# Kernel tuning notes

Measured on AMD Instinct MI355X. Metric: run time of the kernel, lower is better.

## Reference

```python
import jax, jax.numpy as jnp
import numpy as np

N = 100000
E = 800000
D_IN = 64
D_OUT = 64
SCALES = (4, 8)


def setup_inputs() -> dict:
    key = jax.random.key(0)
    ks = jax.random.split(key, 8)
    x = jax.random.normal(ks[0], (N, D_IN), dtype=jnp.float32)
    edge_index = jax.random.randint(ks[1], (2, E), 0, N, dtype=jnp.int64)
    s = 1.0 / np.sqrt(D_IN)
    W1 = jax.random.uniform(ks[2], (D_OUT, D_IN), minval=-s, maxval=s, dtype=jnp.float32)
    b1 = jax.random.uniform(ks[3], (D_OUT,), minval=-s, maxval=s, dtype=jnp.float32)
    W2 = jax.random.uniform(ks[4], (D_OUT, D_IN), minval=-s, maxval=s, dtype=jnp.float32)
    b2 = jax.random.uniform(ks[5], (D_OUT,), minval=-s, maxval=s, dtype=jnp.float32)
    sg = 1.0 / np.sqrt(D_OUT * len(SCALES))
    Wg = jax.random.uniform(ks[6], (D_OUT, D_OUT * len(SCALES)), minval=-sg, maxval=sg, dtype=jnp.float32)
    bg = jax.random.uniform(ks[7], (D_OUT,), minval=-sg, maxval=sg, dtype=jnp.float32)
    return {"x": x, "edge_index": edge_index, "W1": W1, "b1": b1,
            "W2": W2, "b2": b2, "Wg": Wg, "bg": bg}


def _gconv(x, src, tgt, W, b):
    # scatter-add neighbor features: agg[src] += x[tgt]
    agg = jax.ops.segment_sum(x[tgt], src, num_segments=N)  # [N, D_IN]
    counts = jax.ops.segment_sum(jnp.ones((src.shape[0], 1), x.dtype), src,
                                 num_segments=N) + 1e-6     # [N, 1]
    agg = agg / counts
    return agg @ W.T + b                                    # [N, D_OUT]


def reference(x, edge_index, W1, b1, W2, b2, Wg, bg):
    k_max = E // N  # = 8
    outs = []
    for scale, (W, b) in zip(SCALES, ((W1, b1), (W2, b2))):
        scale = min(scale, k_max)
        src = edge_index[0, :N * scale]
        tgt = edge_index[1, :N * scale]
        outs.append(_gconv(x, src, tgt, W, b))
    multi = jnp.concatenate(outs, axis=-1)                   # [N, 2*D_OUT]
    gate = jax.nn.sigmoid(multi @ Wg.T + bg)                 # [N, D_OUT]
    fused = gate * outs[0] + (1.0 - gate) * outs[1]
    return fused
```

## Files before the change

kernel.cpp:

```cpp
#include <hip/hip_runtime.h>
#include <hip/hip_bf16.h>

#define N_NODES 100000
#define E_TOTAL 800000
#define E1      400000
#define D       64
#define CAP     32

#define NPB        128
#define NB         ((N_NODES + NPB - 1) / NPB)
#define BSTRIDE    (NPB * CAP)
#define BCAP       1536
#define EPB        2048
#define NBKT_BLKS  ((E_TOTAL + EPB - 1) / EPB)
#define PREP_TPB   512
#define EPT        (EPB / PREP_TPB)

typedef short s16x8 __attribute__((ext_vector_type(8)));
typedef float f32x4 __attribute__((ext_vector_type(4)));
typedef unsigned u32x4 __attribute__((ext_vector_type(4)));

#define WS_CNT     0
#define WS_ENTRIES (N_NODES)
#define WS_W1B     (WS_ENTRIES + N_NODES * CAP)
#define WS_W2B     (WS_W1B + 2048)
#define WS_WGB     (WS_W2B + 2048)
#define WS_BIAS    (WS_WGB + 4096)
#define WS_CUR     (WS_BIAS + 192)

#define PREP_CONV_BLOCKS 5

__device__ __forceinline__ float ldv(const void* p, size_t idx, int fp32)
{
    return fp32 ? ((const float*)p)[idx]
                : __bfloat162float(((const __hip_bfloat16*)p)[idx]);
}

__device__ __forceinline__ void detect2(const int* ei, const unsigned short* xu,
                                        int* s2, int& e64, int& fp32)
{
    if (threadIdx.x == 0) { s2[0] = 0; s2[1] = 0; }
    __syncthreads();
    if (threadIdx.x < 16 && ei[2 * threadIdx.x + 1] != 0) atomicOr(&s2[0], 1);
    { unsigned u = xu[threadIdx.x]; if (((u >> 7) & 0xFF) >= 0x90) atomicOr(&s2[1], 1); }
    __syncthreads();
    e64 = (s2[0] == 0); fp32 = s2[1];
}

__global__ __launch_bounds__(512) void prep_kernel(
    const void* __restrict__ xv, const int* __restrict__ ei,
    const void* __restrict__ W1v, const void* __restrict__ b1v,
    const void* __restrict__ W2v, const void* __restrict__ b2v,
    const void* __restrict__ Wgv, const void* __restrict__ bgv,
    unsigned* __restrict__ ws)
{
    __shared__ int s2[2];
    __shared__ unsigned hist[NB];
    __shared__ unsigned bbase[NB];
    int e64, fp32;
    detect2(ei, (const unsigned short*)xv, s2, e64, fp32);

    if (blockIdx.x < NBKT_BLKS) {
        for (int j = threadIdx.x; j < NB; j += PREP_TPB) hist[j] = 0;
        __syncthreads();

        const int e0 = blockIdx.x * EPB;
        int srcv[EPT], tgtv[EPT];
#pragma unroll
        for (int i = 0; i < EPT; ++i) {
            const int e = e0 + i * PREP_TPB + threadIdx.x;
            srcv[i] = -1;
            if (e < E_TOTAL) {
                if (e64) {
                    srcv[i] = (int)((const uint2*)ei)[e].x;
                    tgtv[i] = (int)((const uint2*)ei)[E_TOTAL + e].x;
                } else {
                    srcv[i] = ei[e]; tgtv[i] = ei[E_TOTAL + e];
                }
            }
        }
        unsigned recv[EPT], br[EPT];
#pragma unroll
        for (int i = 0; i < EPT; ++i) {
            const int e = e0 + i * PREP_TPB + threadIdx.x;
            br[i] = 0xFFFFFFFFu;
            if (srcv[i] >= 0) {
                const unsigned b = (unsigned)srcv[i] >> 7;
                const unsigned r = atomicAdd(&hist[b], 1u);
                recv[i] = (unsigned)tgtv[i]
                        | ((e < E1) ? 0x20000u : 0u)
                        | (((unsigned)srcv[i] & (NPB - 1)) << 18);
                br[i] = (b << 16) | r;
            }
        }
        __syncthreads();
        for (int j = threadIdx.x; j < NB; j += PREP_TPB) {
            const unsigned h = hist[j];
            bbase[j] = h ? atomicAdd(ws + WS_CUR + j, h) : 0u;
        }
        __syncthreads();
#pragma unroll
        for (int i = 0; i < EPT; ++i) {
            if (br[i] != 0xFFFFFFFFu) {
                const unsigned b = br[i] >> 16, r = br[i] & 0xFFFFu;
                const unsigned pos = bbase[b] + r;
                if (pos < BCAP)
                    ws[WS_ENTRIES + (size_t)b * BSTRIDE + pos] = recv[i];
            }
        }
        return;
    }

    const int gid = (blockIdx.x - NBKT_BLKS) * PREP_TPB + threadIdx.x;
    __hip_bfloat16* W1b = (__hip_bfloat16*)(ws + WS_W1B);
    __hip_bfloat16* W2b = (__hip_bfloat16*)(ws + WS_W2B);
    __hip_bfloat16* Wgb = (__hip_bfloat16*)(ws + WS_WGB);
    float* bias = (float*)(ws + WS_BIAS);

    if (gid < 2048) {
#pragma unroll
        for (int k = 0; k < 8; ++k) {
            const int i = gid * 8 + k;
            if (i < 4096)       W1b[i]        = __float2bfloat16(ldv(W1v, i, fp32));
            else if (i < 8192)  W2b[i - 4096] = __float2bfloat16(ldv(W2v, i - 4096, fp32));
            else                Wgb[i - 8192] = __float2bfloat16(ldv(Wgv, i - 8192, fp32));
        }
    } else if (gid < 2072) {
        const int j = gid - 2048;
#pragma unroll
        for (int k = 0; k < 8; ++k) {
            const int i = j * 8 + k;
            if (i < 64)       bias[i] = ldv(b1v, i, fp32);
            else if (i < 128) bias[i] = ldv(b2v, i - 64, fp32);
            else              bias[i] = ldv(bgv, i - 128, fp32);
        }
    }
}

__global__ __launch_bounds__(256) void csr_kernel(unsigned* __restrict__ ws)
{
    __shared__ unsigned rec_s[BCAP];
    __shared__ __align__(16) unsigned ent[NPB * CAP];
    __shared__ unsigned n1c[NPB], ctc[NPB], a1[NPB], a2[NPB];

    const int b  = blockIdx.x;
    const int n0 = b * NPB;
    const int nn = min(NPB, N_NODES - n0);

    for (int j = threadIdx.x; j < NPB; j += 256) { n1c[j] = 0; ctc[j] = 0; }
    {
        const u32x4 z = {0u, 0u, 0u, 0u};
        for (int j = threadIdx.x; j < NPB * CAP / 4; j += 256) ((u32x4*)ent)[j] = z;
    }
    const unsigned C = min(ws[WS_CUR + b], (unsigned)BCAP);
    for (unsigned r = threadIdx.x; r < C; r += 256)
        rec_s[r] = ws[WS_ENTRIES + (size_t)b * BSTRIDE + r];
    __syncthreads();

    for (unsigned r = threadIdx.x; r < C; r += 256) {
        const unsigned rec = rec_s[r];
        const unsigned sl  = rec >> 18;
        atomicAdd(&ctc[sl], 1u);
        if (rec & 0x20000u) atomicAdd(&n1c[sl], 1u);
    }
    __syncthreads();
    for (int j = threadIdx.x; j < NPB; j += 256) {
        a1[j] = 0u;
        a2[j] = min(n1c[j], (unsigned)CAP);
    }
    __syncthreads();
    for (unsigned r = threadIdx.x; r < C; r += 256) {
        const unsigned rec = rec_s[r];
        const unsigned sl  = rec >> 18;
        unsigned p;
        if (rec & 0x20000u) p = atomicAdd(&a1[sl], 1u);
        else                p = atomicAdd(&a2[sl], 1u);
        if (p < CAP) ent[sl * CAP + p] = rec & 0x1FFFFu;
    }
    __syncthreads();

    const int tot4 = (nn * CAP) / 4;
    u32x4* dst = (u32x4*)(ws + WS_ENTRIES + (size_t)n0 * CAP);
    const u32x4* srcp = (const u32x4*)ent;
    for (int j = threadIdx.x; j < tot4; j += 256) dst[j] = srcp[j];

    if (threadIdx.x < nn) {
        const unsigned ct = min(ctc[threadIdx.x], 0xFFFFu);
        const unsigned p1 = min(n1c[threadIdx.x], (unsigned)CAP);
        ws[WS_CNT + n0 + threadIdx.x] = ct | (p1 << 16);
    }
}

__global__ __launch_bounds__(256) void fused_kernel(
    const unsigned* __restrict__ ws, const void* __restrict__ xv,
    void* __restrict__ outv)
{
    __shared__ __align__(16) __hip_bfloat16 sS[16][136];
    __shared__ __align__(16) __hip_bfloat16 sO[16][136];
    __shared__ int s2d[2];

    if (threadIdx.x == 0) s2d[0] = 0;
    __syncthreads();
    { unsigned u = ((const unsigned short*)xv)[threadIdx.x];
      if (((u >> 7) & 0xFF) >= 0x90) atomicOr(&s2d[0], 1); }
    __syncthreads();
    const int fp32 = s2d[0];

    const int w    = threadIdx.x >> 6;
    const int lane = threadIdx.x & 63;
    const int base = blockIdx.x * 16;

    unsigned entv[4], cw[4];
#pragma unroll
    for (int i = 0; i < 4; ++i) {
        const int n = base + w * 4 + i;
        cw[i]   = ws[WS_CNT + n];
        entv[i] = ws[WS_ENTRIES + (size_t)n * CAP + (lane & 31)];
    }
    int degc[4], p1c[4]; unsigned degt[4];
#pragma unroll
    for (int i = 0; i < 4; ++i) {
        degt[i] = cw[i] & 0xFFFFu;
        p1c[i]  = (int)(cw[i] >> 16);
        degc[i] = (int)min(degt[i], (unsigned)CAP);
    }

    const int half = lane >> 5;
    const int cc   = lane & 31;

    float s1x[4], s1y[4], s2x[4], s2y[4];
#pragma unroll
    for (int i = 0; i < 4; ++i) { s1x[i] = s1y[i] = s2x[i] = s2y[i] = 0.f; }

    int rmax = 0;
#pragma unroll
    for (int i = 0; i < 4; ++i) rmax = max(rmax, (degc[i] + 1) >> 1);
    rmax = (rmax + 3) & ~3;

    if (fp32) {
        const char* xb = (const char*)xv;
        const unsigned ccb = (unsigned)cc << 3;
#pragma unroll 4
        for (int r = 0; r < rmax; ++r) {
#pragma unroll
            for (int i = 0; i < 4; ++i) {
                const int j = 2 * r + half;
                const unsigned en = (unsigned)__shfl((int)entv[i], j);
                const uint2 u = *(const uint2*)(xb + (size_t)((en << 8) + ccb));
                const bool val = j < degc[i];
                const float fx = val ? __uint_as_float(u.x) : 0.f;
                const float fy = val ? __uint_as_float(u.y) : 0.f;
                const float fl = (j < p1c[i]) ? 1.f : 0.f;
                s2x[i] += fx; s2y[i] += fy;
                s1x[i] = fmaf(fl, fx, s1x[i]); s1y[i] = fmaf(fl, fy, s1y[i]);
            }
        }
    } else {
        const char* xb = (const char*)xv;
        const unsigned ccb = (unsigned)cc << 2;
#pragma unroll 4
        for (int r = 0; r < rmax; ++r) {
#pragma unroll
            for (int i = 0; i < 4; ++i) {
                const int j = 2 * r + half;
                const unsigned en = (unsigned)__shfl((int)entv[i], j);
                unsigned u = *(const unsigned*)(xb + (size_t)((en << 7) + ccb));
                u = (j < degc[i]) ? u : 0u;
                const float fx = __uint_as_float(u << 16);
                const float fy = __uint_as_float(u & 0xFFFF0000u);
                const float fl = (j < p1c[i]) ? 1.f : 0.f;
                s2x[i] += fx; s2y[i] += fy;
                s1x[i] = fmaf(fl, fx, s1x[i]); s1y[i] = fmaf(fl, fy, s1y[i]);
            }
        }
    }

#pragma unroll
    for (int i = 0; i < 4; ++i) {
        const int nl = w * 4 + i;
        float a = s1x[i], b = s1y[i], c = s2x[i], d = s2y[i];
        a += __shfl_xor(a, 32); b += __shfl_xor(b, 32);
        c += __shfl_xor(c, 32); d += __shfl_xor(d, 32);
        const float inv1 = 1.0f / ((float)p1c[i] + 1e-6f);
        const float inv2 = 1.0f / ((float)degt[i] + 1e-6f);
        if (lane < 32) {
            const __hip_bfloat162 p1 = __float22bfloat162_rn({a * inv1, b * inv1});
            const __hip_bfloat162 p2 = __float22bfloat162_rn({c * inv2, d * inv2});
            *(__hip_bfloat162*)&sS[nl][2 * cc]      = p1;
            *(__hip_bfloat162*)&sS[nl][64 + 2 * cc] = p2;
        }
    }
    __syncthreads();

    const int m = lane & 15;
    const int q = lane >> 4;
    const int nd = w * 16 + m;

    const s16x8* W1b = (const s16x8*)(ws + WS_W1B);
    const s16x8* W2b = (const s16x8*)(ws + WS_W2B);
    const s16x8* Wgb = (const s16x8*)(ws + WS_WGB);
    const float* bias = (const float*)(ws + WS_BIAS);

    const s16x8 a1c0 = *(const s16x8*)&sS[m][q * 8];
    const s16x8 a1c1 = *(const s16x8*)&sS[m][32 + q * 8];
    const s16x8 a2c0 = *(const s16x8*)&sS[m][64 + q * 8];
    const s16x8 a2c1 = *(const s16x8*)&sS[m][96 + q * 8];

    f32x4 z = {0.f, 0.f, 0.f, 0.f};
    z = __builtin_amdgcn_mfma_f32_16x16x32_bf16(a1c0, W1b[nd * 8 + q],     z, 0, 0, 0);
    z = __builtin_amdgcn_mfma_f32_16x16x32_bf16(a1c1, W1b[nd * 8 + 4 + q], z, 0, 0, 0);
    f32x4 y = {0.f, 0.f, 0.f, 0.f};
    y = __builtin_amdgcn_mfma_f32_16x16x32_bf16(a2c0, W2b[nd * 8 + q],     y, 0, 0, 0);
    y = __builtin_amdgcn_mfma_f32_16x16x32_bf16(a2c1, W2b[nd * 8 + 4 + q], y, 0, 0, 0);
    const float bb1 = bias[nd], bb2 = bias[64 + nd];
#pragma unroll
    for (int r = 0; r < 4; ++r) { z[r] += bb1; y[r] += bb2; }

#pragma unroll
    for (int r = 0; r < 4; ++r) {
        sO[q * 4 + r][nd]      = __float2bfloat16(z[r]);
        sO[q * 4 + r][64 + nd] = __float2bfloat16(y[r]);
    }
    __syncthreads();

    s16x8 ga[4];
#pragma unroll
    for (int c = 0; c < 4; ++c)
        ga[c] = *(const s16x8*)&sO[m][c * 32 + q * 8];

    f32x4 g4 = {0.f, 0.f, 0.f, 0.f};
#pragma unroll
    for (int c = 0; c < 4; ++c)
        g4 = __builtin_amdgcn_mfma_f32_16x16x32_bf16(ga[c], Wgb[nd * 16 + c * 4 + q], g4, 0, 0, 0);
    const float bbg = bias[128 + nd];

#pragma unroll
    for (int r = 0; r < 4; ++r) {
        const float g = 1.0f / (1.0f + __expf(-(g4[r] + bbg)));
        const float v = g * z[r] + (1.0f - g) * y[r];
        const size_t node = (size_t)(base + q * 4 + r);
        if (fp32) ((float*)outv)[node * 64 + nd] = v;
        else      ((__hip_bfloat16*)outv)[node * 64 + nd] = __float2bfloat16(v);
    }
}

extern "C" void kernel_launch(void* const* d_in, const int* in_sizes, int n_in,
                              void* d_out, int out_size, void* d_ws, size_t ws_size,
                              hipStream_t stream)
{
    const void* x  = d_in[0];
    const int*  ei = (const int*)d_in[1];
    unsigned* ws = (unsigned*)d_ws;

    hipMemsetAsync(ws + WS_CUR, 0, 800 * sizeof(unsigned), stream);
    prep_kernel<<<NBKT_BLKS + PREP_CONV_BLOCKS, PREP_TPB, 0, stream>>>(
        x, ei, d_in[2], d_in[3], d_in[4], d_in[5], d_in[6], d_in[7], ws);
    csr_kernel<<<NB, 256, 0, stream>>>(ws);
    fused_kernel<<<N_NODES / 16, 256, 0, stream>>>(ws, x, d_out);
}
```

Before: 165.8 us.

## Pre-convert x to bf16, local-sort bucket writes, and enlarge bucket granularity

Adds a prep stage that converts fp32 x to a bf16 copy in workspace so the gather in the fused kernel reads half the bytes per neighbor. Bucketing now uses 256-node buckets and 4096 edges per block, with an in-block prefix-scan sort in shared memory so global scatter writes are grouped by bucket. Gather loop unrolling drops from 4 to 2, and it falls back to direct fp32 reads when workspace is too small. The cost is an extra full pass over x and more shared memory in prep, and neighbor features are rounded to bf16 before summation, which changes precision.

Measured after the change: 151.4 us. -8.7%, faster.

```diff
diff --git a/kernel.cpp b/kernel.cpp
--- a/kernel.cpp
+++ b/kernel.cpp
@@ -7,14 +7,15 @@
 #define D       64
 #define CAP     32
 
-#define NPB        128
+#define NPB        256
 #define NB         ((N_NODES + NPB - 1) / NPB)
 #define BSTRIDE    (NPB * CAP)
-#define BCAP       1536
-#define EPB        2048
+#define BCAP       3072
+#define EPB        4096
 #define NBKT_BLKS  ((E_TOTAL + EPB - 1) / EPB)
 #define PREP_TPB   512
 #define EPT        (EPB / PREP_TPB)
+#define NBP        512
 
 typedef short s16x8 __attribute__((ext_vector_type(8)));
 typedef float f32x4 __attribute__((ext_vector_type(4)));
@@ -27,8 +28,11 @@
 #define WS_WGB     (WS_W2B + 2048)
 #define WS_BIAS    (WS_WGB + 4096)
 #define WS_CUR     (WS_BIAS + 192)
-
-#define PREP_CONV_BLOCKS 5
+#define WS_XB      (WS_CUR + 512)
+#define WS_NEED_BYTES ((size_t)(WS_XB + (size_t)N_NODES * D / 2) * 4)
+
+#define XCONV_BLOCKS ((N_NODES * D / 16 + PREP_TPB - 1) / PREP_TPB)
+#define WCONV_BLOCKS 5
 
 __device__ __forceinline__ float ldv(const void* p, size_t idx, int fp32)
 {
@@ -52,40 +56,52 @@
     const void* __restrict__ W1v, const void* __restrict__ b1v,
     const void* __restrict__ W2v, const void* __restrict__ b2v,
     const void* __restrict__ Wgv, const void* __restrict__ bgv,
-    unsigned* __restrict__ ws)
+    unsigned* __restrict__ ws, int use_xb)
 {
     __shared__ int s2[2];
     __shared__ unsigned hist[NB];
-    __shared__ unsigned bbase[NB];
+    __shared__ unsigned sc[NBP];
+    __shared__ unsigned gbase[NB];
+    __shared__ unsigned sorted_s[EPB];
+    __shared__ unsigned short bkt_s[EPB];
     int e64, fp32;
     detect2(ei, (const unsigned short*)xv, s2, e64, fp32);
 
+    const int tid = threadIdx.x;
+
     if (blockIdx.x < NBKT_BLKS) {
-        for (int j = threadIdx.x; j < NB; j += PREP_TPB) hist[j] = 0;
+        for (int j = tid; j < NB; j += PREP_TPB) hist[j] = 0;
         __syncthreads();
 
         const int e0 = blockIdx.x * EPB;
         int srcv[EPT], tgtv[EPT];
+        if (e64) {
+#pragma unroll
+            for (int i = 0; i < EPT; ++i) {
+                const int e  = e0 + i * PREP_TPB + tid;
+                const int ec = min(e, E_TOTAL - 1);
+                srcv[i] = (int)((const uint2*)ei)[ec].x;
+                tgtv[i] = (int)((const uint2*)ei)[E_TOTAL + ec].x;
+                if (e >= E_TOTAL) srcv[i] = -1;
+            }
+        } else {
+#pragma unroll
+            for (int i = 0; i < EPT; ++i) {
+                const int e  = e0 + i * PREP_TPB + tid;
+                const int ec = min(e, E_TOTAL - 1);
+                srcv[i] = ei[ec];
+                tgtv[i] = ei[E_TOTAL + ec];
+                if (e >= E_TOTAL) srcv[i] = -1;
+            }
+        }
+
+        unsigned recv[EPT], br[EPT];
 #pragma unroll
         for (int i = 0; i < EPT; ++i) {
-            const int e = e0 + i * PREP_TPB + threadIdx.x;
-            srcv[i] = -1;
-            if (e < E_TOTAL) {
-                if (e64) {
-                    srcv[i] = (int)((const uint2*)ei)[e].x;
-                    tgtv[i] = (int)((const uint2*)ei)[E_TOTAL + e].x;
-                } else {
-                    srcv[i] = ei[e]; tgtv[i] = ei[E_TOTAL + e];
-                }
-            }
-        }
-        unsigned recv[EPT], br[EPT];
-#pragma unroll
-        for (int i = 0; i < EPT; ++i) {
-            const int e = e0 + i * PREP_TPB + threadIdx.x;
+            const int e = e0 + i * PREP_TPB + tid;
             br[i] = 0xFFFFFFFFu;
             if (srcv[i] >= 0) {
-                const unsigned b = (unsigned)srcv[i] >> 7;
+                const unsigned b = (unsigned)srcv[i] >> 8;
                 const unsigned r = atomicAdd(&hist[b], 1u);
                 recv[i] = (unsigned)tgtv[i]
                         | ((e < E1) ? 0x20000u : 0u)
@@ -94,24 +110,68 @@
             }
         }
         __syncthreads();
-        for (int j = threadIdx.x; j < NB; j += PREP_TPB) {
+
+        sc[tid] = (tid < NB) ? hist[tid] : 0u;
+        __syncthreads();
+        for (int s = 1; s < NBP; s <<= 1) {
+            const unsigned v = (tid >= s) ? sc[tid - s] : 0u;
+            __syncthreads();
+            sc[tid] += v;
+            __syncthreads();
+        }
+
+        for (int j = tid; j < NB; j += PREP_TPB) {
             const unsigned h = hist[j];
-            bbase[j] = h ? atomicAdd(ws + WS_CUR + j, h) : 0u;
+            gbase[j] = h ? atomicAdd(ws + WS_CUR + j, h) : 0u;
         }
         __syncthreads();
+
 #pragma unroll
         for (int i = 0; i < EPT; ++i) {
             if (br[i] != 0xFFFFFFFFu) {
                 const unsigned b = br[i] >> 16, r = br[i] & 0xFFFFu;
-                const unsigned pos = bbase[b] + r;
-                if (pos < BCAP)
-                    ws[WS_ENTRIES + (size_t)b * BSTRIDE + pos] = recv[i];
-            }
+                const unsigned pos = (sc[b] - hist[b]) + r;
+                sorted_s[pos] = recv[i];
+                bkt_s[pos] = (unsigned short)b;
+            }
+        }
+        __syncthreads();
+
+        const unsigned tot = sc[NB - 1];
+        for (unsigned k = tid; k < tot; k += PREP_TPB) {
+            const unsigned b = bkt_s[k];
+            const unsigned g = gbase[b] + (k - (sc[b] - hist[b]));
+            if (g < BCAP)
+                ws[WS_ENTRIES + (size_t)b * BSTRIDE + g] = sorted_s[k];
         }
         return;
     }
 
-    const int gid = (blockIdx.x - NBKT_BLKS) * PREP_TPB + threadIdx.x;
+    const int bx = (int)blockIdx.x - NBKT_BLKS;
+    if (bx < XCONV_BLOCKS) {
+        if (use_xb && fp32) {
+            const int gid = bx * PREP_TPB + tid;
+            if (gid < N_NODES * D / 16) {
+                __hip_bfloat16* Xb = (__hip_bfloat16*)(ws + WS_XB);
+                const f32x4* src4 = (const f32x4*)xv + (size_t)gid * 4;
+#pragma unroll
+                for (int h = 0; h < 2; ++h) {
+                    const f32x4 v0 = src4[2 * h];
+                    const f32x4 v1 = src4[2 * h + 1];
+                    s16x8 o;
+#pragma unroll
+                    for (int j = 0; j < 4; ++j) {
+                        o[j]     = (short)__bfloat16_as_ushort(__float2bfloat16(v0[j]));
+                        o[4 + j] = (short)__bfloat16_as_ushort(__float2bfloat16(v1[j]));
+                    }
+                    *(s16x8*)(Xb + (size_t)gid * 16 + h * 8) = o;
+                }
+            }
+        }
+        return;
+    }
+
+    const int gid = (bx - XCONV_BLOCKS) * PREP_TPB + tid;
     __hip_bfloat16* W1b = (__hip_bfloat16*)(ws + WS_W1B);
     __hip_bfloat16* W2b = (__hip_bfloat16*)(ws + WS_W2B);
     __hip_bfloat16* Wgb = (__hip_bfloat16*)(ws + WS_WGB);
@@ -193,7 +253,7 @@
 
 __global__ __launch_bounds__(256) void fused_kernel(
     const unsigned* __restrict__ ws, const void* __restrict__ xv,
-    void* __restrict__ outv)
+    void* __restrict__ outv, int use_xb)
 {
     __shared__ __align__(16) __hip_bfloat16 sS[16][136];
     __shared__ __align__(16) __hip_bfloat16 sO[16][136];
@@ -235,12 +295,31 @@
     int rmax = 0;
 #pragma unroll
     for (int i = 0; i < 4; ++i) rmax = max(rmax, (degc[i] + 1) >> 1);
-    rmax = (rmax + 3) & ~3;
-
-    if (fp32) {
+    rmax = (rmax + 1) & ~1;
+
+    const int direct_f32 = (fp32 && !use_xb);
+    if (!direct_f32) {
+        const char* xb = fp32 ? (const char*)(ws + WS_XB) : (const char*)xv;
+        const unsigned ccb = (unsigned)cc << 2;
+#pragma unroll 2
+        for (int r = 0; r < rmax; ++r) {
+#pragma unroll
+            for (int i = 0; i < 4; ++i) {
+                const int j = 2 * r + half;
+                const unsigned en = (unsigned)__shfl((int)entv[i], j);
+                unsigned u = *(const unsigned*)(xb + (size_t)((en << 7) + ccb));
+                u = (j < degc[i]) ? u : 0u;
+                const float fx = __uint_as_float(u << 16);
+                const float fy = __uint_as_float(u & 0xFFFF0000u);
+                const float fl = (j < p1c[i]) ? 1.f : 0.f;
+                s2x[i] += fx; s2y[i] += fy;
+                s1x[i] = fmaf(fl, fx, s1x[i]); s1y[i] = fmaf(fl, fy, s1y[i]);
+            }
+        }
+    } else {
         const char* xb = (const char*)xv;
         const unsigned ccb = (unsigned)cc << 3;
-#pragma unroll 4
+#pragma unroll 2
         for (int r = 0; r < rmax; ++r) {
 #pragma unroll
             for (int i = 0; i < 4; ++i) {
@@ -250,24 +329,6 @@
                 const bool val = j < degc[i];
                 const float fx = val ? __uint_as_float(u.x) : 0.f;
                 const float fy = val ? __uint_as_float(u.y) : 0.f;
-                const float fl = (j < p1c[i]) ? 1.f : 0.f;
-                s2x[i] += fx; s2y[i] += fy;
-                s1x[i] = fmaf(fl, fx, s1x[i]); s1y[i] = fmaf(fl, fy, s1y[i]);
-            }
-        }
-    } else {
-        const char* xb = (const char*)xv;
-        const unsigned ccb = (unsigned)cc << 2;
-#pragma unroll 4
-        for (int r = 0; r < rmax; ++r) {
-#pragma unroll
-            for (int i = 0; i < 4; ++i) {
-                const int j = 2 * r + half;
-                const unsigned en = (unsigned)__shfl((int)entv[i], j);
-                unsigned u = *(const unsigned*)(xb + (size_t)((en << 7) + ccb));
-                u = (j < degc[i]) ? u : 0u;
-                const float fx = __uint_as_float(u << 16);
-                const float fy = __uint_as_float(u & 0xFFFF0000u);
                 const float fl = (j < p1c[i]) ? 1.f : 0.f;
                 s2x[i] += fx; s2y[i] += fy;
                 s1x[i] = fmaf(fl, fx, s1x[i]); s1y[i] = fmaf(fl, fy, s1y[i]);
@@ -352,9 +413,11 @@
     const int*  ei = (const int*)d_in[1];
     unsigned* ws = (unsigned*)d_ws;
 
-    hipMemsetAsync(ws + WS_CUR, 0, 800 * sizeof(unsigned), stream);
-    prep_kernel<<<NBKT_BLKS + PREP_CONV_BLOCKS, PREP_TPB, 0, stream>>>(
-        x, ei, d_in[2], d_in[3], d_in[4], d_in[5], d_in[6], d_in[7], ws);
+    const int use_xb = (ws_size >= WS_NEED_BYTES) ? 1 : 0;
+
+    hipMemsetAsync(ws + WS_CUR, 0, NB * sizeof(unsigned), stream);
+    prep_kernel<<<NBKT_BLKS + XCONV_BLOCKS + WCONV_BLOCKS, PREP_TPB, 0, stream>>>(
+        x, ei, d_in[2], d_in[3], d_in[4], d_in[5], d_in[6], d_in[7], ws, use_xb);
     csr_kernel<<<NB, 256, 0, stream>>>(ws);
-    fused_kernel<<<N_NODES / 16, 256, 0, stream>>>(ws, x, d_out);
-}
+    fused_kernel<<<N_NODES / 16, 256, 0, stream>>>(ws, x, d_out, use_xb);
+}
```
